# Optimization experiments

Hardware: AMD Instinct MI355X
Metric: run time of the kernel (lower is better)

Reference implementation:

```python
import jax, jax.numpy as jnp
import numpy as np
import math

EMB_S = 64
HEADS = 8
EMB = EMB_S * HEADS  # 512
M = int(EMB_S * 0.5)  # 32 random features
B, T = 8, 4096
EPS = 1e-5


def setup_inputs() -> dict:
    key = jax.random.key(0)
    ks = jax.random.split(key, 16)
    s_in = 1.0 / math.sqrt(EMB_S)
    s_emb = 1.0 / math.sqrt(EMB)
    s_hid = 1.0 / math.sqrt(4 * EMB)
    return {
        "x": jax.random.normal(ks[0], (B, T, EMB), jnp.float32),
        "w": jax.random.normal(ks[1], (M, EMB_S), jnp.float32),  # frozen random features
        "kqv_w": jax.random.uniform(ks[2], (3 * EMB_S, EMB_S), jnp.float32, -s_in, s_in),
        "kqv_b": jax.random.uniform(ks[3], (3 * EMB_S,), jnp.float32, -s_in, s_in),
        "proj_w": jax.random.uniform(ks[4], (EMB, EMB), jnp.float32, -s_emb, s_emb),
        "proj_b": jax.random.uniform(ks[5], (EMB,), jnp.float32, -s_emb, s_emb),
        "ln1_g": 1.0 + 0.02 * jax.random.normal(ks[6], (EMB,), jnp.float32),
        "ln1_b": 0.02 * jax.random.normal(ks[7], (EMB,), jnp.float32),
        "ln2_g": 1.0 + 0.02 * jax.random.normal(ks[8], (EMB,), jnp.float32),
        "ln2_b": 0.02 * jax.random.normal(ks[9], (EMB,), jnp.float32),
        "mlp_w1": jax.random.uniform(ks[10], (4 * EMB, EMB), jnp.float32, -s_emb, s_emb),
        "mlp_b1": jax.random.uniform(ks[11], (4 * EMB,), jnp.float32, -s_emb, s_emb),
        "mlp_w2": jax.random.uniform(ks[12], (EMB, 4 * EMB), jnp.float32, -s_hid, s_hid),
        "mlp_b2": jax.random.uniform(ks[13], (EMB,), jnp.float32, -s_hid, s_hid),
    }


def _layer_norm(x, g, b):
    mu = jnp.mean(x, axis=-1, keepdims=True)
    var = jnp.mean(jnp.square(x - mu), axis=-1, keepdims=True)
    return (x - mu) * jax.lax.rsqrt(var + EPS) * g + b


def _prm_exp(z, w):
    # z: [B,T,H,E]; softmax-kernel random features, [B,T,H,M]
    xd = 0.5 * jnp.sum(z * z, axis=-1, keepdims=True)
    wtx = jnp.einsum("bthe,me->bthm", z, w)
    return jnp.exp(wtx - xd) / math.sqrt(M)


def reference(x, w, kqv_w, kqv_b, proj_w, proj_b, ln1_g, ln1_b, ln2_g, ln2_b,
              mlp_w1, mlp_b1, mlp_w2, mlp_b2):
    Bb, Tt, _ = x.shape
    h = _layer_norm(x, ln1_g, ln1_b).reshape(Bb, Tt, HEADS, EMB_S)
    kqv = jnp.einsum("bthe,fe->bthf", h, kqv_w) + kqv_b  # [B,T,H,3E]
    k, q, v = jnp.split(kqv, 3, axis=-1)  # torch.split order: k, q, v
    kp = _prm_exp(k, w)  # [B,T,H,M]
    qp = _prm_exp(q, w)
    D = jnp.einsum("bthm,bhm->bth", qp, kp.sum(axis=1))  # [B,T,H]
    kptv = jnp.einsum("bthe,bthm->bhem", v, kp)  # [B,H,E,M]
    y = jnp.einsum("bthm,bhem->bthe", qp, kptv) / D[..., None]
    y = y.reshape(Bb, Tt, EMB)
    attn = jnp.einsum("btf,ef->bte", y, proj_w) + proj_b  # dropout = identity (eval)
    x = x + attn
    h2 = _layer_norm(x, ln2_g, ln2_b)
    hid = jax.nn.gelu(jnp.einsum("bte,fe->btf", h2, mlp_w1) + mlp_b1, approximate=False)
    mlp_out = jnp.einsum("btf,ef->bte", hid, mlp_w2) + mlp_b2
    return x + mlp_out
```

## Files before the change

kernel.cpp:

```cpp
#include <hip/hip_runtime.h>
#include <hip/hip_bf16.h>

typedef __bf16 bf16x8_t __attribute__((ext_vector_type(8)));
typedef float f32x4_t __attribute__((ext_vector_type(4)));
using bf16 = __hip_bfloat16;

#define EMB 512
#define NTOK 32768
#define NROW 262144
#define SQRT_M_INV 0.17677669529663687f
#define KNC 16

__device__ __forceinline__ void gload16(const void* g, void* l) {
  __builtin_amdgcn_global_load_lds((const __attribute__((address_space(1))) void*)g,
                                   (__attribute__((address_space(3))) void*)l, 16, 0, 0);
}

__device__ __forceinline__ float fast_gelu(float v) {
  float u = v * 0.70710678118654752f;
  float a = fabsf(u);
  float tt = __builtin_amdgcn_rcpf(fmaf(0.3275911f, a, 1.0f));
  float p = fmaf(tt, 1.061405429f, -1.453152027f);
  p = fmaf(tt, p, 1.421413741f);
  p = fmaf(tt, p, -0.284496736f);
  p = fmaf(tt, p, 0.254829592f);
  p = p * tt;
  float e = __expf(-a * a);
  float er = fmaf(-p, e, 1.0f);
  er = copysignf(er, u);
  return 0.5f * v * (1.0f + er);
}

__device__ __forceinline__ void cvt4(const float* __restrict__ in,
                                     bf16* __restrict__ out, int i4, int n4) {
  if (i4 < n4) {
    float4 v = ((const float4*)in)[i4];
    alignas(8) bf16 o[4];
    o[0] = __float2bfloat16(v.x); o[1] = __float2bfloat16(v.y);
    o[2] = __float2bfloat16(v.z); o[3] = __float2bfloat16(v.w);
    *(uint2*)(out + i4 * 4) = *(const uint2*)o;
  }
}
__global__ __launch_bounds__(256) void f2b4_kernel(
    const float* __restrict__ a, bf16* __restrict__ oa, int na4,
    const float* __restrict__ b, bf16* __restrict__ ob, int nb4,
    const float* __restrict__ c, bf16* __restrict__ oc, int nc4,
    const float* __restrict__ d, bf16* __restrict__ od, int nd4) {
  int i4 = blockIdx.x * 256 + threadIdx.x;
  cvt4(a, oa, i4, na4);
  cvt4(b, ob, i4, nb4);
  cvt4(c, oc, i4, nc4);
  cvt4(d, od, i4, nd4);
}

__global__ __launch_bounds__(256) void ln_kernel(const float* __restrict__ x,
                                                 const float* __restrict__ g,
                                                 const float* __restrict__ bt,
                                                 bf16* __restrict__ out) {
  int lane = threadIdx.x & 63;
  int row = blockIdx.x * 4 + (threadIdx.x >> 6);
  const float* xr = x + (size_t)row * EMB;
  float4 v0 = ((const float4*)xr)[lane * 2];
  float4 v1 = ((const float4*)xr)[lane * 2 + 1];
  float s = v0.x + v0.y + v0.z + v0.w + v1.x + v1.y + v1.z + v1.w;
#pragma unroll
  for (int o = 32; o; o >>= 1) s += __shfl_xor(s, o);
  float mu = s * (1.0f / 512.0f);
  float vs = 0.f, d;
  d = v0.x - mu; vs += d * d;  d = v0.y - mu; vs += d * d;
  d = v0.z - mu; vs += d * d;  d = v0.w - mu; vs += d * d;
  d = v1.x - mu; vs += d * d;  d = v1.y - mu; vs += d * d;
  d = v1.z - mu; vs += d * d;  d = v1.w - mu; vs += d * d;
#pragma unroll
  for (int o = 32; o; o >>= 1) vs += __shfl_xor(vs, o);
  float rstd = rsqrtf(vs * (1.0f / 512.0f) + 1e-5f);
  float4 g0 = ((const float4*)g)[lane * 2], g1 = ((const float4*)g)[lane * 2 + 1];
  float4 b0 = ((const float4*)bt)[lane * 2], b1 = ((const float4*)bt)[lane * 2 + 1];
  alignas(16) bf16 o8[8];
  o8[0] = __float2bfloat16((v0.x - mu) * rstd * g0.x + b0.x);
  o8[1] = __float2bfloat16((v0.y - mu) * rstd * g0.y + b0.y);
  o8[2] = __float2bfloat16((v0.z - mu) * rstd * g0.z + b0.z);
  o8[3] = __float2bfloat16((v0.w - mu) * rstd * g0.w + b0.w);
  o8[4] = __float2bfloat16((v1.x - mu) * rstd * g1.x + b1.x);
  o8[5] = __float2bfloat16((v1.y - mu) * rstd * g1.y + b1.y);
  o8[6] = __float2bfloat16((v1.z - mu) * rstd * g1.z + b1.z);
  o8[7] = __float2bfloat16((v1.w - mu) * rstd * g1.w + b1.w);
  *(uint4*)(out + (size_t)row * EMB + lane * 8) = *(const uint4*)o8;
}

template <int BM, int BN, int WM, int WN, int OP>
__global__ __launch_bounds__(256) void gemm_bt(const bf16* __restrict__ A,
                                               const bf16* __restrict__ W,
                                               const float* __restrict__ bias,
                                               const float* __restrict__ res,
                                               float* __restrict__ outF,
                                               bf16* __restrict__ outB,
                                               int M, int N, int K) {
  constexpr int BK = 32;
  constexpr int TM = BM / WM, TN = BN / WN;
  constexpr int NI = TM / 16, NJ = TN / 16;
  constexpr int AP = BM * BK / 2048;
  constexpr int WP = BN * BK / 2048;
  alignas(16) __shared__ bf16 As[2][BM * BK];
  alignas(16) __shared__ bf16 Ws[2][BN * BK];
  int t = threadIdx.x;
  int lane = t & 63, wid = t >> 6;
  int wm = wid % WM, wn = wid / WM;
  int nwg = gridDim.x * gridDim.y;
  int lin = blockIdx.y * gridDim.x + blockIdx.x;
  if ((nwg & 7) == 0) lin = (lin & 7) * (nwg >> 3) + (lin >> 3);
  int bn = (lin % gridDim.x) * BN, bm = (lin / gridDim.x) * BM;
  int lr = lane & 15, lq = lane >> 4;
  const int r0 = (t * 8) >> 5, c0 = (t * 8) & 31;

  const bf16* ap = A + (size_t)(bm + r0) * K + c0;
  const bf16* wp = W + (size_t)(bn + r0) * K + c0;
  const size_t strA = (size_t)64 * K;

  f32x4_t acc[NI][NJ];
#pragma unroll
  for (int i = 0; i < NI; ++i)
#pragma unroll
    for (int j = 0; j < NJ; ++j)
#pragma unroll
      for (int r = 0; r < 4; ++r) acc[i][j][r] = 0.f;

  auto stage = [&](int buf) {
#pragma unroll
    for (int p = 0; p < AP; ++p)
      gload16(ap + (size_t)p * strA, &As[buf][(r0 + p * 64) * BK + c0]);
#pragma unroll
    for (int p = 0; p < WP; ++p)
      gload16(wp + (size_t)p * strA, &Ws[buf][(r0 + p * 64) * BK + c0]);
    ap += BK;
    wp += BK;
  };
  auto compute = [&](int buf) {
    bf16x8_t afr[NI], bfr[NJ];
#pragma unroll
    for (int i = 0; i < NI; ++i)
      afr[i] = *(const bf16x8_t*)&As[buf][(wm * TM + i * 16 + lr) * BK + lq * 8];
#pragma unroll
    for (int j = 0; j < NJ; ++j)
      bfr[j] = *(const bf16x8_t*)&Ws[buf][(wn * TN + j * 16 + lr) * BK + lq * 8];
#pragma unroll
    for (int i = 0; i < NI; ++i)
#pragma unroll
      for (int j = 0; j < NJ; ++j)
        acc[i][j] = __builtin_amdgcn_mfma_f32_16x16x32_bf16(afr[i], bfr[j], acc[i][j], 0, 0, 0);
  };

  const int nt = K / BK;
  stage(0);
  int cur = 0;
  for (int kt = 0; kt < nt - 1; ++kt) {
    __syncthreads();
    stage(cur ^ 1);
    compute(cur);
    cur ^= 1;
  }
  __syncthreads();
  compute(cur);

#pragma unroll
  for (int i = 0; i < NI; ++i)
#pragma unroll
    for (int j = 0; j < NJ; ++j) {
      int gn = bn + wn * TN + j * 16 + lr;
      float bv = bias[gn];
#pragma unroll
      for (int r = 0; r < 4; ++r) {
        int gm = bm + wm * TM + i * 16 + lq * 4 + r;
        float v = acc[i][j][r] + bv;
        size_t off = (size_t)gm * N + gn;
        if (OP == 0) {
          outF[off] = v;
        } else if (OP == 1) {
          outF[off] = v + res[off];
        } else {
          outB[off] = __float2bfloat16(fast_gelu(v));
        }
      }
    }
}

__device__ __forceinline__ size_t bh_row(size_t grow) {
  size_t h = grow & 7, bt = grow >> 3;
  size_t b = bt >> 12, tt = bt & 4095;
  return ((b * 8 + h) << 12) + tt;
}

__global__ __launch_bounds__(256) void kqv_prm_kernel(
    const bf16* __restrict__ A,
    const bf16* __restrict__ Wk,
    const float* __restrict__ bias,
    const float* __restrict__ wrf,
    float* __restrict__ kp, float* __restrict__ qp,
    bf16* __restrict__ vout) {
  constexpr int LDZ = 136;
  constexpr int LDV = 72;
  alignas(16) __shared__ char u_raw[27648];
  bf16* As  = (bf16*)u_raw;
  bf16* Ws  = (bf16*)(u_raw + 4096);
  bf16* zkq = (bf16*)u_raw;
  bf16* vs  = (bf16*)(u_raw + 17408);
  float* xd_s = (float*)(u_raw + 26624);

  int t = threadIdx.x;
  int lane = t & 63, wid = t >> 6;
  int wm = wid & 1, wn = wid >> 1;
  int lr = lane & 15, lq = lane >> 4;
  size_t row0 = (size_t)blockIdx.x * 64;

  bf16x8_t wfrag[2][2];
#pragma unroll
  for (int mt = 0; mt < 2; ++mt)
#pragma unroll
    for (int ks = 0; ks < 2; ++ks) {
      const float* src = wrf + (mt * 16 + lr) * 64 + ks * 32 + lq * 8;
#pragma unroll
      for (int jj = 0; jj < 8; ++jj) wfrag[mt][ks][jj] = (__bf16)src[jj];
    }

  f32x4_t acc[2][6];
#pragma unroll
  for (int i = 0; i < 2; ++i)
#pragma unroll
    for (int j = 0; j < 6; ++j)
#pragma unroll
      for (int r = 0; r < 4; ++r) acc[i][j][r] = 0.f;

  const int r0 = t >> 2, c0 = (t * 8) & 31;
  for (int k0 = 0; k0 < 64; k0 += 32) {
    gload16(&A[(row0 + r0) * 64 + k0 + c0], &As[r0 * 32 + c0]);
#pragma unroll
    for (int p = 0; p < 3; ++p) {
      int r = r0 + p * 64;
      gload16(&Wk[(size_t)r * 64 + k0 + c0], &Ws[r * 32 + c0]);
    }
    __syncthreads();
    bf16x8_t af[2], bfr[6];
#pragma unroll
    for (int i = 0; i < 2; ++i)
      af[i] = *(const bf16x8_t*)&As[(wm * 32 + i * 16 + lr) * 32 + lq * 8];
#pragma unroll
    for (int j = 0; j < 6; ++j)
      bfr[j] = *(const bf16x8_t*)&Ws[(wn * 96 + j * 16 + lr) * 32 + lq * 8];
#pragma unroll
    for (int i = 0; i < 2; ++i)
#pragma unroll
      for (int j = 0; j < 6; ++j)
        acc[i][j] = __builtin_amdgcn_mfma_f32_16x16x32_bf16(af[i], bfr[j], acc[i][j], 0, 0, 0);
    __syncthreads();
  }

#pragma unroll
  for (int i = 0; i < 2; ++i)
#pragma unroll
    for (int j = 0; j < 6; ++j) {
      int col = wn * 96 + j * 16 + lr;
      float bv = bias[col];
      int rowb = wm * 32 + i * 16 + lq * 4;
#pragma unroll
      for (int r = 0; r < 4; ++r) {
        float v = acc[i][j][r] + bv;
        if (col < 128) zkq[(rowb + r) * LDZ + col] = __float2bfloat16(v);
        else           vs[(rowb + r) * LDV + (col - 128)] = __float2bfloat16(v);
      }
    }
  __syncthreads();

  if (t < 128) {
    int r = t & 63, sel = t >> 6;
    const bf16* zr = &zkq[r * LDZ + sel * 64];
    float xd = 0.f;
#pragma unroll
    for (int c = 0; c < 64; c += 8) {
      bf16x8_t z8 = *(const bf16x8_t*)&zr[c];
#pragma unroll
      for (int jj = 0; jj < 8; ++jj) { float f = (float)z8[jj]; xd += f * f; }
    }
    xd_s[r * 2 + sel] = 0.5f * xd;
  }
  __syncthreads();

#pragma unroll
  for (int p = 0; p < 2; ++p) {
    int idx = t + p * 256;
    int r = idx >> 3, c8 = idx & 7;
    size_t nr = bh_row(row0 + r);
    *(uint4*)&vout[nr * 64 + c8 * 8] = *(const uint4*)&vs[r * LDV + c8 * 8];
  }

  int sel = wn;
  f32x4_t aw[2][2];
#pragma unroll
  for (int i = 0; i < 2; ++i)
#pragma unroll
    for (int mt = 0; mt < 2; ++mt)
#pragma unroll
      for (int r = 0; r < 4; ++r) aw[i][mt][r] = 0.f;
#pragma unroll
  for (int ks = 0; ks < 2; ++ks) {
    bf16x8_t af2[2];
#pragma unroll
    for (int i = 0; i < 2; ++i)
      af2[i] = *(const bf16x8_t*)&zkq[(wm * 32 + i * 16 + lr) * LDZ + sel * 64 + ks * 32 + lq * 8];
#pragma unroll
    for (int i = 0; i < 2; ++i)
#pragma unroll
      for (int mt = 0; mt < 2; ++mt)
        aw[i][mt] = __builtin_amdgcn_mfma_f32_16x16x32_bf16(af2[i], wfrag[mt][ks], aw[i][mt], 0, 0, 0);
  }
  float* outp = sel ? qp : kp;
#pragma unroll
  for (int i = 0; i < 2; ++i)
#pragma unroll
    for (int r = 0; r < 4; ++r) {
      int row = wm * 32 + i * 16 + lq * 4 + r;
      size_t nr = bh_row(row0 + row);
#pragma unroll
      for (int mt = 0; mt < 2; ++mt) {
        int m = mt * 16 + lr;
        outp[nr * 32 + m] =
            __expf(aw[i][mt][r] - xd_s[row * 2 + sel]) * SQRT_M_INV;
      }
    }
}

__global__ __launch_bounds__(256) void kptv_kernel(const bf16* __restrict__ v2,
                                                   const float* __restrict__ kp2,
                                                   float* __restrict__ part) {
  int bh = blockIdx.x, chunk = blockIdx.y;
  int t = threadIdx.x;
  int ts = t >> 6;
  int eg = (t >> 2) & 15;
  int g  = t & 3;
  const int T0 = chunk * 256;
  const bf16* vp = v2 + ((size_t)bh * 4096 + T0) * 64 + eg * 4;
  const float* kpp = kp2 + ((size_t)bh * 4096 + T0) * 32 + g * 8;

  float acc[4][8];
  float accs[8];
#pragma unroll
  for (int e = 0; e < 4; ++e)
#pragma unroll
    for (int m = 0; m < 8; ++m) acc[e][m] = 0.f;
#pragma unroll
  for (int m = 0; m < 8; ++m) accs[m] = 0.f;

#pragma unroll 2
  for (int tok = ts; tok < 256; tok += 4) {
    union { uint2 u; ushort s[4]; } vr;
    vr.u = *(const uint2*)(vp + (size_t)tok * 64);
    float ve[4];
#pragma unroll
    for (int e = 0; e < 4; ++e)
      ve[e] = __uint_as_float((uint32_t)vr.s[e] << 16);
    float4 k0 = *(const float4*)(kpp + (size_t)tok * 32);
    float4 k1 = *(const float4*)(kpp + (size_t)tok * 32 + 4);
    float km[8] = {k0.x, k0.y, k0.z, k0.w, k1.x, k1.y, k1.z, k1.w};
#pragma unroll
    for (int e = 0; e < 4; ++e)
#pragma unroll
      for (int m = 0; m < 8; ++m) acc[e][m] = fmaf(ve[e], km[m], acc[e][m]);
#pragma unroll
    for (int m = 0; m < 8; ++m) accs[m] += km[m];
  }

  __shared__ float red[256][33];
  __shared__ float reds[4][4][8];
#pragma unroll
  for (int e = 0; e < 4; ++e)
#pragma unroll
    for (int m = 0; m < 8; ++m) red[t][e * 8 + m] = acc[e][m];
  if (eg == 0) {
#pragma unroll
    for (int m = 0; m < 8; ++m) reds[ts][g][m] = accs[m];
  }
  __syncthreads();

  int l = t >> 2, q = t & 3;
  int leg = l >> 2, lg = l & 3;
  float o[8];
#pragma unroll
  for (int m = 0; m < 8; ++m)
    o[m] = red[l][q * 8 + m] + red[l + 64][q * 8 + m] +
           red[l + 128][q * 8 + m] + red[l + 192][q * 8 + m];
  float* pp = part + (size_t)(bh * KNC + chunk) * 2080 + (leg * 4 + q) * 32 + lg * 8;
  *(float4*)pp = make_float4(o[0], o[1], o[2], o[3]);
  *(float4*)(pp + 4) = make_float4(o[4], o[5], o[6], o[7]);
  if (t < 32) {
    int g2 = t >> 3, j = t & 7;
    float s = reds[0][g2][j] + reds[1][g2][j] + reds[2][g2][j] + reds[3][g2][j];
    part[(size_t)(bh * KNC + chunk) * 2080 + 2048 + g2 * 8 + j] = s;
  }
}

__global__ __launch_bounds__(256) void y_kernel(const float* __restrict__ qp2,
                                                const float* __restrict__ part,
                                                bf16* __restrict__ y) {
  int bh = blockIdx.x, chunk = blockIdx.y;
  int b = bh >> 3, h = bh & 7;
  alignas(16) __shared__ float qp_s[16][32];
  int t = threadIdx.x;
  int e = t & 63, iq = t >> 6;
  float kv[32], ks[32];
#pragma unroll
  for (int m = 0; m < 32; ++m) { kv[m] = 0.f; ks[m] = 0.f; }
  for (int c = 0; c < KNC; ++c) {
    const float* pp = part + (size_t)(bh * KNC + c) * 2080;
#pragma unroll
    for (int m = 0; m < 32; m += 4) {
      float4 a = *(const float4*)&pp[e * 32 + m];
      kv[m] += a.x; kv[m + 1] += a.y; kv[m + 2] += a.z; kv[m + 3] += a.w;
      float4 s = *(const float4*)&pp[2048 + m];
      ks[m] += s.x; ks[m + 1] += s.y; ks[m + 2] += s.z; ks[m + 3] += s.w;
    }
  }
  for (int grp = 0; grp < 32; ++grp) {
    int tok0 = chunk * 512 + grp * 16;
    __syncthreads();
    if (t < 128) {
      int r = t >> 3, c4 = t & 7;
      *(float4*)&qp_s[r][c4 * 4] =
          *(const float4*)(qp2 + ((size_t)bh * 4096 + tok0 + r) * 32 + c4 * 4);
    }
    __syncthreads();
#pragma unroll
    for (int i0 = 0; i0 < 4; ++i0) {
      int i = iq * 4 + i0;
      float dot = 0.f, dd = 0.f;
#pragma unroll
      for (int m = 0; m < 32; m += 4) {
        float4 qq = *(const float4*)&qp_s[i][m];
        dot += qq.x * kv[m] + qq.y * kv[m + 1] + qq.z * kv[m + 2] + qq.w * kv[m + 3];
        dd  += qq.x * ks[m] + qq.y * ks[m + 1] + qq.z * ks[m + 2] + qq.w * ks[m + 3];
      }
      y[(size_t)(b * 4096 + tok0 + i) * EMB + h * 64 + e] = __float2bfloat16(dot / dd);
    }
  }
}

extern "C" void kernel_launch(void* const* d_in, const int* in_sizes, int n_in,
                              void* d_out, int out_size, void* d_ws, size_t ws_size,
                              hipStream_t stream) {
  const float* x      = (const float*)d_in[0];
  const float* w      = (const float*)d_in[1];
  const float* kqv_w  = (const float*)d_in[2];
  const float* kqv_b  = (const float*)d_in[3];
  const float* proj_w = (const float*)d_in[4];
  const float* proj_b = (const float*)d_in[5];
  const float* ln1_g  = (const float*)d_in[6];
  const float* ln1_b  = (const float*)d_in[7];
  const float* ln2_g  = (const float*)d_in[8];
  const float* ln2_b  = (const float*)d_in[9];
  const float* mlp_w1 = (const float*)d_in[10];
  const float* mlp_b1 = (const float*)d_in[11];
  const float* mlp_w2 = (const float*)d_in[12];
  const float* mlp_b2 = (const float*)d_in[13];
  float* out = (float*)d_out;

  char* ws = (char*)d_ws;
  size_t off = 0;
  auto alloc = [&](size_t bytes) -> void* {
    void* p = ws + off;
    off = (off + bytes + 255) & ~(size_t)255;
    return p;
  };

  bf16* kqv_wb  = (bf16*)alloc(12288 * 2);
  bf16* proj_wb = (bf16*)alloc(262144 * 2);
  bf16* w1b     = (bf16*)alloc(1048576 * 2);
  bf16* w2b     = (bf16*)alloc(1048576 * 2);
  bf16* hb      = (bf16*)alloc((size_t)NTOK * EMB * 2);
  bf16* yb      = hb;
  float* qpb    = (float*)alloc((size_t)NROW * 32 * 4);
  bf16* h2b     = (bf16*)qpb;
  float* kpb    = (float*)alloc((size_t)NROW * 32 * 4);
  bf16* hidb    = (bf16*)kpb;
  bf16* vb      = (bf16*)alloc((size_t)NROW * 64 * 2);
  float* partb  = (float*)alloc((size_t)64 * KNC * 2080 * 4);

  f2b4_kernel<<<1024, 256, 0, stream>>>(kqv_w, kqv_wb, 12288 / 4,
                                        proj_w, proj_wb, 262144 / 4,
                                        mlp_w1, w1b, 1048576 / 4,
                                        mlp_w2, w2b, 1048576 / 4);

  ln_kernel<<<NTOK / 4, 256, 0, stream>>>(x, ln1_g, ln1_b, hb);

  kqv_prm_kernel<<<NROW / 64, 256, 0, stream>>>(hb, kqv_wb, kqv_b, w, kpb, qpb, vb);

  kptv_kernel<<<dim3(64, KNC), 256, 0, stream>>>(vb, kpb, partb);

  y_kernel<<<dim3(64, 8), 256, 0, stream>>>(qpb, partb, yb);

  gemm_bt<128, 128, 2, 2, 1><<<dim3(4, NTOK / 128), 256, 0, stream>>>(
      yb, proj_wb, proj_b, x, out, nullptr, NTOK, 512, 512);

  ln_kernel<<<NTOK / 4, 256, 0, stream>>>(out, ln2_g, ln2_b, h2b);

  for (int c = 0; c < 2; ++c) {
    const bf16* h2c = h2b + (size_t)c * 16384 * 512;
    float* outc = out + (size_t)c * 16384 * 512;
    gemm_bt<128, 128, 2, 2, 2><<<dim3(16, 128), 256, 0, stream>>>(
        h2c, w1b, mlp_b1, nullptr, nullptr, hidb, 16384, 2048, 512);
    gemm_bt<64, 128, 1, 4, 1><<<dim3(4, 256), 256, 0, stream>>>(
        hidb, w2b, mlp_b2, outc, outc, nullptr, 16384, 512, 2048);
  }
}
```

Before: 604.0 us.

## Restructure y_kernel with shared reduction, precomputed normalizer and double-buffered qp loads

The kernel that combines the random-feature query with the per-head key-value sums is reorganised in three ways. The per-chunk partial sums are now reduced cooperatively into shared memory, with each thread summing 8 elements. Before, every thread redundantly summed 64 values across all chunks. The denominator 1/(qp·ksum) is computed once per token up front and stored in shared memory, instead of being recomputed for each of the 64 output columns. Query rows are fetched with async global-to-LDS loads into a double buffer, and output stores are deferred by one group so each group needs only one barrier. The costs are extra shared memory and reliance on the barrier to wait for the async loads to complete.

```diff
diff --git a/kernel.cpp b/kernel.cpp
--- a/kernel.cpp
+++ b/kernel.cpp
@@ -402,43 +402,99 @@
                                                 bf16* __restrict__ y) {
   int bh = blockIdx.x, chunk = blockIdx.y;
   int b = bh >> 3, h = bh & 7;
-  alignas(16) __shared__ float qp_s[16][32];
+  __shared__ float kv_s[64][36];
+  __shared__ float ks_s[32];
+  __shared__ float inv_dd[512];
+  alignas(16) __shared__ float qp_s[2][16][32];
   int t = threadIdx.x;
   int e = t & 63, iq = t >> 6;
-  float kv[32], ks[32];
-#pragma unroll
-  for (int m = 0; m < 32; ++m) { kv[m] = 0.f; ks[m] = 0.f; }
-  for (int c = 0; c < KNC; ++c) {
-    const float* pp = part + (size_t)(bh * KNC + c) * 2080;
-#pragma unroll
-    for (int m = 0; m < 32; m += 4) {
-      float4 a = *(const float4*)&pp[e * 32 + m];
-      kv[m] += a.x; kv[m + 1] += a.y; kv[m + 2] += a.z; kv[m + 3] += a.w;
-      float4 s = *(const float4*)&pp[2048 + m];
-      ks[m] += s.x; ks[m + 1] += s.y; ks[m + 2] += s.z; ks[m + 3] += s.w;
-    }
-  }
+  const int T0 = chunk * 512;
+  const size_t qbase = (size_t)bh * 4096 + T0;
+
+  {
+    int er = t >> 2, m0 = (t & 3) * 8;
+    float4 a0 = make_float4(0.f, 0.f, 0.f, 0.f);
+    float4 a1 = make_float4(0.f, 0.f, 0.f, 0.f);
+#pragma unroll 4
+    for (int c = 0; c < KNC; ++c) {
+      const float* pp = part + (size_t)(bh * KNC + c) * 2080 + er * 32 + m0;
+      float4 u = *(const float4*)pp;
+      float4 v = *(const float4*)(pp + 4);
+      a0.x += u.x; a0.y += u.y; a0.z += u.z; a0.w += u.w;
+      a1.x += v.x; a1.y += v.y; a1.z += v.z; a1.w += v.w;
+    }
+    *(float4*)&kv_s[er][m0] = a0;
+    *(float4*)&kv_s[er][m0 + 4] = a1;
+    if (t < 32) {
+      float s = 0.f;
+#pragma unroll 4
+      for (int c = 0; c < KNC; ++c)
+        s += part[(size_t)(bh * KNC + c) * 2080 + 2048 + t];
+      ks_s[t] = s;
+    }
+  }
+  __syncthreads();
+
+  float kv[32];
+#pragma unroll
+  for (int m = 0; m < 32; m += 4) *(float4*)&kv[m] = *(const float4*)&kv_s[e][m];
+
+  if (t < 128)
+    gload16(qp2 + (qbase + (t >> 3)) * 32 + (t & 7) * 4,
+            &qp_s[0][t >> 3][(t & 7) * 4]);
+
+  {
+    float ks[32];
+#pragma unroll
+    for (int m = 0; m < 32; m += 4) *(float4*)&ks[m] = *(const float4*)&ks_s[m];
+#pragma unroll
+    for (int p = 0; p < 2; ++p) {
+      int tok = t + p * 256;
+      const float* qrow = qp2 + (qbase + tok) * 32;
+      float dd = 0.f;
+#pragma unroll
+      for (int m = 0; m < 32; m += 4) {
+        float4 qq = *(const float4*)&qrow[m];
+        dd += qq.x * ks[m] + qq.y * ks[m + 1] + qq.z * ks[m + 2] + qq.w * ks[m + 3];
+      }
+      inv_dd[tok] = 1.0f / dd;
+    }
+  }
+
+  float dreg[4];
+  int cur = 0;
   for (int grp = 0; grp < 32; ++grp) {
-    int tok0 = chunk * 512 + grp * 16;
     __syncthreads();
-    if (t < 128) {
-      int r = t >> 3, c4 = t & 7;
-      *(float4*)&qp_s[r][c4 * 4] =
-          *(const float4*)(qp2 + ((size_t)bh * 4096 + tok0 + r) * 32 + c4 * 4);
-    }
-    __syncthreads();
+    if (grp > 0) {
+      int tokp = (grp - 1) * 16 + iq * 4;
+#pragma unroll
+      for (int i0 = 0; i0 < 4; ++i0)
+        y[(size_t)(b * 4096 + T0 + tokp + i0) * EMB + h * 64 + e] =
+            __float2bfloat16(dreg[i0]);
+    }
+    if (grp < 31 && t < 128) {
+      int nr = (grp + 1) * 16;
+      gload16(qp2 + (qbase + nr + (t >> 3)) * 32 + (t & 7) * 4,
+              &qp_s[cur ^ 1][t >> 3][(t & 7) * 4]);
+    }
 #pragma unroll
     for (int i0 = 0; i0 < 4; ++i0) {
       int i = iq * 4 + i0;
-      float dot = 0.f, dd = 0.f;
+      float dot = 0.f;
 #pragma unroll
       for (int m = 0; m < 32; m += 4) {
-        float4 qq = *(const float4*)&qp_s[i][m];
+        float4 qq = *(const float4*)&qp_s[cur][i][m];
         dot += qq.x * kv[m] + qq.y * kv[m + 1] + qq.z * kv[m + 2] + qq.w * kv[m + 3];
-        dd  += qq.x * ks[m] + qq.y * ks[m + 1] + qq.z * ks[m + 2] + qq.w * ks[m + 3];
       }
-      y[(size_t)(b * 4096 + tok0 + i) * EMB + h * 64 + e] = __float2bfloat16(dot / dd);
-    }
+      dreg[i0] = dot * inv_dd[grp * 16 + i];
+    }
+    cur ^= 1;
+  }
+#pragma unroll
+  for (int i0 = 0; i0 < 4; ++i0) {
+    int tokp = 31 * 16 + iq * 4 + i0;
+    y[(size_t)(b * 4096 + T0 + tokp) * EMB + h * 64 + e] =
+        __float2bfloat16(dreg[i0]);
   }
 }
 
```

After: 578.7 us. 1.04x faster.
